# Kernel optimization log

Measured on AMD Instinct MI355X. Metric: run time of the kernel, lower is better.

## Reference

```python
import jax, jax.numpy as jnp
import numpy as np

DIM = 192
TDIM = 192
HEADS = 6
WS = (2, 7, 7)
SS = (1, 3, 3)
MLP_HID = 4 * DIM
RANK = DIM // 8
EPS = 1e-6


def _rel_pos_index(ws):
    wd, wh, ww = ws
    coords = np.stack(np.meshgrid(np.arange(wd), np.arange(wh), np.arange(ww), indexing='ij'))
    cf = coords.reshape(3, -1)
    rel = (cf[:, :, None] - cf[:, None, :]).transpose(1, 2, 0).astype(np.int64)
    rel[..., 0] += wd - 1
    rel[..., 1] += wh - 1
    rel[..., 2] += ww - 1
    rel[..., 0] *= (2 * wh - 1) * (2 * ww - 1)
    rel[..., 1] *= (2 * ww - 1)
    return rel.sum(-1)  # (N, N)


def _window_partition(x, ws):
    B, D, H, W, C = x.shape
    x = x.reshape(B, D // ws[0], ws[0], H // ws[1], ws[1], W // ws[2], ws[2], C)
    return x.transpose(0, 1, 3, 5, 2, 4, 6, 7).reshape(-1, ws[0] * ws[1] * ws[2], C)


def _window_reverse(w, ws, B, D, H, W):
    x = w.reshape(B, D // ws[0], H // ws[1], W // ws[2], ws[0], ws[1], ws[2], -1)
    return x.transpose(0, 1, 4, 2, 5, 3, 6, 7).reshape(B, D, H, W, -1)


def _ln(x):
    m = x.mean(-1, keepdims=True)
    v = ((x - m) ** 2).mean(-1, keepdims=True)
    return (x - m) * jax.lax.rsqrt(v + EPS)


def _compute_mask_np(Dp, Hp, Wp, ws, ss):
    img = np.zeros((1, Dp, Hp, Wp, 1), dtype=np.float32)
    cnt = 0
    for d in (slice(0, -ws[0]), slice(-ws[0], -ss[0]), slice(-ss[0], None)):
        for h in (slice(0, -ws[1]), slice(-ws[1], -ss[1]), slice(-ss[1], None)):
            for w in (slice(0, -ws[2]), slice(-ws[2], -ss[2]), slice(-ss[2], None)):
                img[:, d, h, w, :] = cnt
                cnt += 1
    x = img.reshape(1, Dp // ws[0], ws[0], Hp // ws[1], ws[1], Wp // ws[2], ws[2], 1)
    mw = x.transpose(0, 1, 3, 5, 2, 4, 6, 7).reshape(-1, ws[0] * ws[1] * ws[2])
    am = mw[:, None, :] - mw[:, :, None]
    return np.where(am != 0, np.float32(-100.0), np.float32(0.0))


def setup_inputs() -> dict:
    key = jax.random.key(0)
    ks = jax.random.split(key, 16)
    B, D, H, W, C = 1, 16, 64, 128, DIM
    Dp = D + (-D) % WS[0]
    Hp = H + (-H) % WS[1]
    Wp = W + (-W) % WS[2]
    s = 0.02
    bias_tab = (2 * WS[0] - 1) * (2 * WS[1] - 1) * (2 * WS[2] - 1)
    return {
        'x': jax.random.normal(ks[0], (B, D, H, W, C), jnp.float32),
        'mask_matrix': jnp.asarray(_compute_mask_np(Dp, Hp, Wp, WS, SS)),
        't': jax.random.normal(ks[1], (B, TDIM), jnp.float32),
        'w_qkv': jax.random.normal(ks[2], (C, 3 * C), jnp.float32) * s,
        'b_qkv': jnp.zeros((3 * C,), jnp.float32),
        'rel_bias': jax.random.normal(ks[3], (bias_tab, HEADS), jnp.float32) * s,
        'w_proj': jax.random.normal(ks[4], (C, C), jnp.float32) * s,
        'b_proj': jnp.zeros((C,), jnp.float32),
        'w1': jax.random.normal(ks[5], (C, MLP_HID), jnp.float32) * s,
        'b1': jnp.zeros((MLP_HID,), jnp.float32),
        'w2': jax.random.normal(ks[6], (MLP_HID, C), jnp.float32) * s,
        'b2': jnp.zeros((C,), jnp.float32),
        'wa1': jax.random.normal(ks[7], (TDIM, RANK), jnp.float32) * s,
        'wa2': jax.random.normal(ks[8], (RANK, 6 * C), jnp.float32) * s,
        'ba2': jax.random.normal(ks[9], (6 * C,), jnp.float32) * s,
    }


def reference(x, mask_matrix, t, w_qkv, b_qkv, rel_bias, w_proj, b_proj, w1, b1, w2, b2, wa1, wa2, ba2):
    B, D, H, W, C = x.shape
    hd = C // HEADS
    # AdaLN modulation params
    mod = (jax.nn.silu(t) @ wa1) @ wa2 + ba2  # (B, 6C)
    sh_msa, sc_msa, g_msa, sh_mlp, sc_mlp, g_mlp = jnp.split(mod, 6, axis=1)

    def modulate(y, sh, sc):
        return y * (1 + sc[:, None, None, None, :]) + sh[:, None, None, None, :]

    shortcut = x
    y = modulate(_ln(x), sh_msa, sc_msa)
    # pad to window multiples
    pad_d, pad_h, pad_w = (-D) % WS[0], (-H) % WS[1], (-W) % WS[2]
    y = jnp.pad(y, ((0, 0), (0, pad_d), (0, pad_h), (0, pad_w), (0, 0)))
    Dp, Hp, Wp = D + pad_d, H + pad_h, W + pad_w
    # cyclic shift
    y = jnp.roll(y, (-SS[0], -SS[1], -SS[2]), axis=(1, 2, 3))
    xw = _window_partition(y, WS)  # (B*nW, N, C)
    N = xw.shape[1]
    qkv = (xw @ w_qkv + b_qkv).reshape(-1, N, 3, HEADS, hd)
    q, k, v = qkv[:, :, 0], qkv[:, :, 1], qkv[:, :, 2]
    scale = hd ** -0.5
    attn = jnp.einsum('bnhd,bmhd->bhnm', q * scale, k)  # (B*nW, H, N, N)
    rpi = _rel_pos_index(WS)
    bias = rel_bias[rpi.reshape(-1)].reshape(N, N, HEADS).transpose(2, 0, 1)
    attn = attn + bias[None]
    nW = mask_matrix.shape[0]
    attn = attn.reshape(B, nW, HEADS, N, N) + mask_matrix[None, :, None]
    attn = jax.nn.softmax(attn, axis=-1).reshape(-1, HEADS, N, N)
    out = jnp.einsum('bhnm,bmhd->bnhd', attn, v).reshape(-1, N, C)
    out = out @ w_proj + b_proj
    y = _window_reverse(out, WS, B, Dp, Hp, Wp)
    y = jnp.roll(y, (SS[0], SS[1], SS[2]), axis=(1, 2, 3))
    y = y[:, :D, :H, :W, :]
    x1 = shortcut + g_msa[:, None, None, None, :] * y
    y2 = modulate(_ln(x1), sh_mlp, sc_mlp)
    h = jax.nn.gelu(y2 @ w1 + b1, approximate=False) @ w2 + b2
    return x1 + g_mlp[:, None, None, None, :] * h
```

## Files before the change

kernel.cpp:

```cpp
#include <hip/hip_runtime.h>
#include <hip/hip_bf16.h>

typedef __bf16 bf16x8 __attribute__((ext_vector_type(8)));
typedef float  f32x4  __attribute__((ext_vector_type(4)));
typedef unsigned int u32x4 __attribute__((ext_vector_type(4)));

__device__ inline unsigned short f2bf(float f) {
    union { __hip_bfloat16 h; unsigned short u; } cv;
    cv.h = __float2bfloat16(f);
    return cv.u;
}
__device__ inline float bf2f(unsigned short u) {
    union { unsigned int i; float f; } c; c.i = ((unsigned int)u) << 16; return c.f;
}

__device__ inline bf16x8 load8(const unsigned short* p) {
    uint2 lo = *(const uint2*)(p);
    uint2 hi = *(const uint2*)(p + 16);
    u32x4 v; v[0] = lo.x; v[1] = lo.y; v[2] = hi.x; v[3] = hi.y;
    return __builtin_bit_cast(bf16x8, v);
}

__device__ inline f32x4 mfma16(bf16x8 a, bf16x8 b, f32x4 c) {
    return __builtin_amdgcn_mfma_f32_16x16x32_bf16(a, b, c, 0, 0, 0);
}

__device__ inline bool winmapT(int gg, int& T) {
    int win = gg / 98, n = gg % 98;
    int wdi = win / 190, rem = win % 190, whi = rem / 19, wwi = rem % 19;
    int td = n / 49, th = (n / 7) % 7, tw = n % 7;
    int sd = (wdi * 2 + td + 1) & 15;
    int sh = whi * 7 + th + 3; if (sh >= 70) sh -= 70;
    int sw = wwi * 7 + tw + 3; if (sw >= 133) sw -= 133;
    if (sh < 64 && sw < 128) { T = (sd * 64 + sh) * 128 + sw; return true; }
    return false;
}

__global__ __launch_bounds__(256) void mod_k(const float* __restrict__ t,
    const float* __restrict__ wa1, const float* __restrict__ wa2,
    const float* __restrict__ ba2, float* __restrict__ mod)
{
    __shared__ float st[192];
    __shared__ float a[24];
    int tid = threadIdx.x;
    if (tid < 192) { float x = t[tid]; st[tid] = x / (1.f + __expf(-x)); }
    __syncthreads();
    if (tid < 24) {
        float s = 0.f;
        for (int c = 0; c < 192; ++c) s += st[c] * wa1[c * 24 + tid];
        a[tid] = s;
    }
    __syncthreads();
    for (int j = tid; j < 1152; j += 256) {
        float s = ba2[j];
        for (int r = 0; r < 24; ++r) s += a[r] * wa2[r * 1152 + j];
        mod[j] = s;
    }
}

__global__ __launch_bounds__(256) void prep_k(
    const float* __restrict__ wqkv, const float* __restrict__ wproj,
    const float* __restrict__ w1, const float* __restrict__ w2,
    const float* __restrict__ relb,
    unsigned short* __restrict__ wqkvT, unsigned short* __restrict__ wprojT,
    unsigned short* __restrict__ w1T, unsigned short* __restrict__ w2T,
    unsigned short* __restrict__ btabF)
{
    int i = blockIdx.x * 256 + threadIdx.x;
    if (i < 110592) { int n = i / 192, k = i % 192; wqkvT[i] = f2bf(wqkv[k * 576 + n]); return; }
    i -= 110592;
    if (i < 36864)  { int n = i / 192, k = i % 192; wprojT[i] = f2bf(wproj[k * 192 + n]); return; }
    i -= 36864;
    if (i < 147456) { int n = i / 192, k = i % 192; w1T[i] = f2bf(w1[k * 768 + n]); return; }
    i -= 147456;
    if (i < 147456) { int n = i / 768, k = i % 768; w2T[i] = f2bf(w2[k * 192 + n]); return; }
    i -= 147456;
    if (i < 688128) {
        int mt = i / 86016, r1 = i % 86016;
        int h  = r1 / 14336, r2 = r1 % 14336;
        int fm = r2 / 2048,  r3 = r2 % 2048;
        int le = r3 / 128,   r4 = r3 % 128;
        int l16 = r4 / 8,    fn = r4 % 8;
        int r = fm * 16 + le, c = fn * 16 + l16;
        float val;
        if (fn == 7 || r >= 98 || c >= 98) {
            val = -1e30f;
        } else {
            int tdn = r / 49, thn = (r / 7) % 7, twn = r % 7;
            int tdm = c / 49, thm = (c / 7) % 7, twm = c % 7;
            int idx = (tdn - tdm + 1) * 169 + (thn - thm + 6) * 13 + (twn - twm + 6);
            float b = relb[idx * 6 + h];
            int bd = mt & 1, bh = (mt >> 1) & 1, bw = (mt >> 2) & 1;
            int idn = (bd ? (tdn == 0 ? 1 : 2) : 0) * 9 + (bh ? (thn < 4 ? 1 : 2) : 0) * 3 + (bw ? (twn < 4 ? 1 : 2) : 0);
            int idm = (bd ? (tdm == 0 ? 1 : 2) : 0) * 9 + (bh ? (thm < 4 ? 1 : 2) : 0) * 3 + (bw ? (twm < 4 ? 1 : 2) : 0);
            val = b + ((idn != idm) ? -100.f : 0.f);
        }
        btabF[i] = f2bf(val);
    }
}

__global__ __launch_bounds__(256) void stats_f32_k(const float* __restrict__ x,
    float* __restrict__ st)
{
    int tok = blockIdx.x * 4 + (threadIdx.x >> 6);
    int lane = threadIdx.x & 63;
    const float* p = x + (size_t)tok * 192;
    float a = p[lane], b = p[64 + lane], c = p[128 + lane];
    float s = a + b + c, q = a * a + b * b + c * c;
    for (int m = 32; m; m >>= 1) { s += __shfl_xor(s, m); q += __shfl_xor(q, m); }
    if (lane == 0) {
        float mean = s * (1.f / 192.f);
        float var  = q * (1.f / 192.f) - mean * mean;
        st[2 * tok] = mean;
        st[2 * tok + 1] = rsqrtf(var + 1e-6f);
    }
}

template<int FN, int STAGE, int EPI>
__global__ __launch_bounds__(256) void gemm_k(
    const unsigned short* __restrict__ A, const float* __restrict__ Af,
    const unsigned short* __restrict__ BT, const float* __restrict__ bias,
    unsigned short* __restrict__ outB, float* outF,
    const float* __restrict__ auxF, const float* __restrict__ stats,
    const float* __restrict__ mod, int row0, int M, int N, int K)
{
    constexpr int BN = FN * 32;
    __shared__ unsigned short As[128][44];
    __shared__ unsigned short Bs[BN][44];
    const int t = threadIdx.x;
    const int n0 = blockIdx.x * BN, m0 = blockIdx.y * 128;
    const int lr = t >> 2, lk = (t & 3) * 8;
    const int wid = t >> 6, lane = t & 63;
    const int lg = lane >> 4, l16 = lane & 15;
    const int wm = (wid >> 1) * 64, wn = (wid & 1) * (FN * 16);
    f32x4 acc[4][FN] = {};

    float mn[2] = {0.f, 0.f}, rs[2] = {0.f, 0.f};
    size_t sbase[2] = {0, 0};
    bool va[2] = {false, false};
    #pragma unroll
    for (int rr = 0; rr < 2; ++rr) {
        int g = m0 + lr + rr * 64;
        if (STAGE == 1) {
            int T;
            if (g < M && winmapT(row0 + g, T)) {
                va[rr] = true; sbase[rr] = (size_t)T * 192;
                mn[rr] = stats[2 * T]; rs[rr] = stats[2 * T + 1];
            }
        } else if (STAGE == 2) {
            int tok = row0 + g;
            sbase[rr] = (size_t)tok * 192;
            mn[rr] = stats[2 * tok]; rs[rr] = stats[2 * tok + 1];
        }
    }

    for (int kk = 0; kk < K; kk += 32) {
        #pragma unroll
        for (int rr = 0; rr < 2; ++rr) {
            int r = lr + rr * 64;
            int g = m0 + r;
            uint4 w = make_uint4(0u, 0u, 0u, 0u);
            if (STAGE == 0) {
                if (g < M) w = *(const uint4*)(A + (size_t)g * K + kk + lk);
            } else if (STAGE == 1) {
                if (va[rr]) {
                    float4 xa = *(const float4*)(Af + sbase[rr] + kk + lk);
                    float4 xb = *(const float4*)(Af + sbase[rr] + kk + lk + 4);
                    float xs[8] = {xa.x, xa.y, xa.z, xa.w, xb.x, xb.y, xb.z, xb.w};
                    unsigned short o[8];
                    #pragma unroll
                    for (int j = 0; j < 8; ++j) {
                        int c = kk + lk + j;
                        o[j] = f2bf((xs[j] - mn[rr]) * rs[rr] * (1.f + mod[192 + c]) + mod[c]);
                    }
                    w = make_uint4((unsigned)o[0] | ((unsigned)o[1] << 16), (unsigned)o[2] | ((unsigned)o[3] << 16),
                                   (unsigned)o[4] | ((unsigned)o[5] << 16), (unsigned)o[6] | ((unsigned)o[7] << 16));
                }
            } else {
                float4 xa = *(const float4*)(Af + sbase[rr] + kk + lk);
                float4 xb = *(const float4*)(Af + sbase[rr] + kk + lk + 4);
                float xs[8] = {xa.x, xa.y, xa.z, xa.w, xb.x, xb.y, xb.z, xb.w};
                unsigned short o[8];
                #pragma unroll
                for (int j = 0; j < 8; ++j) {
                    int c = kk + lk + j;
                    o[j] = f2bf((xs[j] - mn[rr]) * rs[rr] * (1.f + mod[768 + c]) + mod[576 + c]);
                }
                w = make_uint4((unsigned)o[0] | ((unsigned)o[1] << 16), (unsigned)o[2] | ((unsigned)o[3] << 16),
                               (unsigned)o[4] | ((unsigned)o[5] << 16), (unsigned)o[6] | ((unsigned)o[7] << 16));
            }
            *(uint2*)(&As[r][lk])     = make_uint2(w.x, w.y);
            *(uint2*)(&As[r][lk + 4]) = make_uint2(w.z, w.w);
        }
        #pragma unroll
        for (int rr = 0; rr < BN / 64; ++rr) {
            int r = lr + rr * 64;
            int gn = n0 + r;
            uint4 w = make_uint4(0u, 0u, 0u, 0u);
            if (gn < N) w = *(const uint4*)(BT + (size_t)gn * K + kk + lk);
            *(uint2*)(&Bs[r][lk])     = make_uint2(w.x, w.y);
            *(uint2*)(&Bs[r][lk + 4]) = make_uint2(w.z, w.w);
        }
        __syncthreads();
        bf16x8 af[4], bv[FN];
        #pragma unroll
        for (int i = 0; i < 4; ++i) af[i] = load8(&As[wm + i * 16 + l16][4 * lg]);
        #pragma unroll
        for (int j = 0; j < FN; ++j) bv[j] = load8(&Bs[wn + j * 16 + l16][4 * lg]);
        #pragma unroll
        for (int i = 0; i < 4; ++i)
        #pragma unroll
        for (int j = 0; j < FN; ++j)
            acc[i][j] = mfma16(af[i], bv[j], acc[i][j]);
        __syncthreads();
    }

    #pragma unroll
    for (int i = 0; i < 4; ++i)
    #pragma unroll
    for (int j = 0; j < FN; ++j) {
        int gcol = n0 + wn + j * 16 + l16;
        if (gcol >= N) continue;
        float b = bias[gcol];
        #pragma unroll
        for (int e = 0; e < 4; ++e) {
            int grow = m0 + wm + i * 16 + lg * 4 + e;
            if (grow >= M) continue;
            float v = acc[i][j][e] + b;
            if (EPI == 0) {
                outB[(size_t)grow * N + gcol] = f2bf(v);
            } else if (EPI == 1) {
                float gl = 0.5f * v * (1.f + erff(v * 0.70710678118654752f));
                outB[(size_t)grow * N + gcol] = f2bf(gl);
            } else if (EPI == 2) {
                int T;
                if (winmapT(row0 + grow, T)) {
                    size_t idx = (size_t)T * 192 + gcol;
                    outF[idx] = auxF[idx] + mod[384 + gcol] * v;
                }
            } else {
                size_t idx = (size_t)(row0 + grow) * 192 + gcol;
                outF[idx] = outF[idx] + mod[960 + gcol] * v;
            }
        }
    }
}

__global__ __launch_bounds__(256) void attn_k(
    const unsigned short* __restrict__ qkv, const unsigned short* __restrict__ btabF,
    unsigned short* __restrict__ out)
{
    __shared__ __align__(16) char smem[40896];
    unsigned short* Qs  = (unsigned short*)smem;
    unsigned short* Ks  = (unsigned short*)(smem + 9856);
    unsigned short* Pbf = (unsigned short*)smem;
    unsigned short* VT  = (unsigned short*)(smem + 31808);

    const int blk = blockIdx.x;
    const int win = blk / 6, h = blk % 6;
    const int t = threadIdx.x;
    const int wid = t >> 6, lg = (t >> 4) & 3, l16 = t & 15;
    const size_t rb = (size_t)win * 98;

    const int wdi = win / 190, remw = win % 190, whi = remw / 19, wwi = remw % 19;
    const int mt = (wdi == 7 ? 1 : 0) | (whi == 9 ? 2 : 0) | (wwi == 18 ? 4 : 0);
    const unsigned short* btF = btabF + (size_t)(mt * 6 + h) * 14336;

    uint4 vreg[2];
    const int vi0 = t, vi1 = t + 256;
    if (vi0 < 392) vreg[0] = *(const uint4*)(qkv + (rb + (vi0 >> 2)) * 576 + 384 + h * 32 + (vi0 & 3) * 8);
    if (vi1 < 392) vreg[1] = *(const uint4*)(qkv + (rb + (vi1 >> 2)) * 576 + 384 + h * 32 + (vi1 & 3) * 8);

    for (int i = t; i < 98 * 4; i += 256) {
        int r = i >> 2, cg = (i & 3) * 8;
        uint4 q = *(const uint4*)(qkv + (rb + r) * 576 + h * 32 + cg);
        uint4 k = *(const uint4*)(qkv + (rb + r) * 576 + 192 + h * 32 + cg);
        *(uint2*)(Qs + r * 44 + cg)     = make_uint2(q.x, q.y);
        *(uint2*)(Qs + r * 44 + cg + 4) = make_uint2(q.z, q.w);
        *(uint2*)(Ks + r * 44 + cg)     = make_uint2(k.x, k.y);
        *(uint2*)(Ks + r * 44 + cg + 4) = make_uint2(k.z, k.w);
    }
    for (int i = t; i < 14 * 32; i += 256) {
        int r = 98 + (i >> 5), c = i & 31;
        Qs[r * 44 + c] = 0; Ks[r * 44 + c] = 0;
    }
    __syncthreads();

    f32x4 acc[2][7];
    {
        bf16x8 kb[7];
        #pragma unroll
        for (int fn = 0; fn < 7; ++fn) kb[fn] = load8(Ks + (fn * 16 + l16) * 44 + 4 * lg);
        #pragma unroll
        for (int fi = 0; fi < 2; ++fi) {
            int fm = wid + fi * 4;
            if (fm < 7) {
                bf16x8 qa = load8(Qs + (fm * 16 + l16) * 44 + 4 * lg);
                #pragma unroll
                for (int fn = 0; fn < 7; ++fn) {
                    f32x4 z = {};
                    acc[fi][fn] = mfma16(qa, kb[fn], z);
                }
            }
        }
    }
    __syncthreads();

    uint4 btreg[2][4];
    #pragma unroll
    for (int fi = 0; fi < 2; ++fi) {
        int fm = wid + fi * 4;
        int fmc = (fm < 7) ? fm : 0;
        #pragma unroll
        for (int e = 0; e < 4; ++e)
            btreg[fi][e] = *(const uint4*)(btF + fmc * 2048 + (lg * 4 + e) * 128 + l16 * 8);
    }
    {
        if (vi0 < 392) {
            int m = vi0 >> 2, c0 = (vi0 & 3) * 8;
            const unsigned short* vp = (const unsigned short*)&vreg[0];
            #pragma unroll
            for (int j = 0; j < 8; ++j) VT[(c0 + j) * 142 + m] = vp[j];
        }
        if (vi1 < 392) {
            int m = vi1 >> 2, c0 = (vi1 & 3) * 8;
            const unsigned short* vp = (const unsigned short*)&vreg[1];
            #pragma unroll
            for (int j = 0; j < 8; ++j) VT[(c0 + j) * 142 + m] = vp[j];
        }
    }
    for (int i = t; i < 32 * 30; i += 256) { int c = i / 30, m = 98 + i % 30; VT[c * 142 + m] = 0; }
    for (int i = t; i < 112 * 8; i += 256) {
        int r = i >> 3, cc = 112 + (i & 7) * 2;
        *(unsigned int*)(Pbf + r * 142 + cc) = 0u;
    }

    const float SCALE = 0.17677669529663687f;
    float rinv[2][4];
    #pragma unroll
    for (int fi = 0; fi < 2; ++fi) {
        int fm = wid + fi * 4;
        if (fm < 7) {
            #pragma unroll
            for (int e = 0; e < 4; ++e) {
                const unsigned int bw[4] = {btreg[fi][e].x, btreg[fi][e].y, btreg[fi][e].z, btreg[fi][e].w};
                float mx = -1e30f;
                #pragma unroll
                for (int fn = 0; fn < 7; ++fn) {
                    unsigned short bu = (unsigned short)(bw[fn >> 1] >> ((fn & 1) * 16));
                    float s = fmaf(acc[fi][fn][e], SCALE, bf2f(bu));
                    acc[fi][fn][e] = s;
                    mx = fmaxf(mx, s);
                }
                #pragma unroll
                for (int m = 1; m < 16; m <<= 1) mx = fmaxf(mx, __shfl_xor(mx, m));
                float sum = 0.f;
                #pragma unroll
                for (int fn = 0; fn < 7; ++fn) {
                    float p = __expf(acc[fi][fn][e] - mx);
                    acc[fi][fn][e] = p;
                    sum += p;
                }
                #pragma unroll
                for (int m = 1; m < 16; m <<= 1) sum += __shfl_xor(sum, m);
                rinv[fi][e] = 1.f / sum;
            }
            #pragma unroll
            for (int fn = 0; fn < 7; ++fn) {
                int c = fn * 16 + l16;
                #pragma unroll
                for (int e = 0; e < 4; ++e) {
                    int r = fm * 16 + lg * 4 + e;
                    Pbf[r * 142 + c] = f2bf(acc[fi][fn][e]);
                }
            }
        }
    }
    __syncthreads();

    #pragma unroll
    for (int fi = 0; fi < 2; ++fi) {
        int fm = wid + fi * 4;
        if (fm < 7) {
            bf16x8 sa[4];
            #pragma unroll
            for (int ks = 0; ks < 4; ++ks)
                sa[ks] = load8(Pbf + (fm * 16 + l16) * 142 + ks * 32 + 4 * lg);
            #pragma unroll
            for (int fn = 0; fn < 2; ++fn) {
                f32x4 o = {};
                #pragma unroll
                for (int ks = 0; ks < 4; ++ks) {
                    bf16x8 vb = load8(VT + (fn * 16 + l16) * 142 + ks * 32 + 4 * lg);
                    o = mfma16(sa[ks], vb, o);
                }
                #pragma unroll
                for (int e = 0; e < 4; ++e) {
                    int r = fm * 16 + lg * 4 + e;
                    if (r < 98) {
                        out[(rb + r) * 192 + h * 32 + fn * 16 + l16] = f2bf(o[e] * rinv[fi][e]);
                    }
                }
            }
        }
    }
}

extern "C" void kernel_launch(void* const* d_in, const int* in_sizes, int n_in,
                              void* d_out, int out_size, void* d_ws, size_t ws_size,
                              hipStream_t stream)
{
    const float* x      = (const float*)d_in[0];
    const float* tvec   = (const float*)d_in[2];
    const float* w_qkv  = (const float*)d_in[3];
    const float* b_qkv  = (const float*)d_in[4];
    const float* relb   = (const float*)d_in[5];
    const float* w_proj = (const float*)d_in[6];
    const float* b_proj = (const float*)d_in[7];
    const float* w1     = (const float*)d_in[8];
    const float* b1     = (const float*)d_in[9];
    const float* w2     = (const float*)d_in[10];
    const float* b2     = (const float*)d_in[11];
    const float* wa1    = (const float*)d_in[12];
    const float* wa2    = (const float*)d_in[13];
    const float* ba2    = (const float*)d_in[14];

    char* ws = (char*)d_ws;
    float*          mod    = (float*)ws;
    float*          stats1 = (float*)(ws + 4608);
    float*          stats2 = (float*)(ws + 1053184);
    unsigned short* wqkvT  = (unsigned short*)(ws + 2101760);
    unsigned short* wprojT = (unsigned short*)(ws + 2322944);
    unsigned short* w1T    = (unsigned short*)(ws + 2396672);
    unsigned short* w2T    = (unsigned short*)(ws + 2691584);
    unsigned short* btabF  = (unsigned short*)(ws + 2986496);
    unsigned short* qkvb   = (unsigned short*)(ws + 4834304);
    unsigned short* h      = (unsigned short*)(ws + 4834304);
    unsigned short* attn_c = (unsigned short*)(ws + 176436224);
    float*          dout   = (float*)d_out;

    mod_k<<<1, 256, 0, stream>>>(tvec, wa1, wa2, ba2, mod);
    prep_k<<<4416, 256, 0, stream>>>(w_qkv, w_proj, w1, w2, relb, wqkvT, wprojT, w1T, w2T, btabF);
    stats_f32_k<<<32768, 256, 0, stream>>>(x, stats1);

    gemm_k<4, 1, 0><<<dim3(5, 1164), 256, 0, stream>>>(
        nullptr, x, wqkvT, b_qkv, qkvb, nullptr, nullptr, stats1, mod, 0, 148960, 576, 192);
    attn_k<<<9120, 256, 0, stream>>>(qkvb, btabF, attn_c);
    gemm_k<2, 0, 2><<<dim3(3, 1164), 256, 0, stream>>>(
        attn_c, nullptr, wprojT, b_proj, nullptr, dout, x, nullptr, mod, 0, 148960, 192, 192);

    stats_f32_k<<<32768, 256, 0, stream>>>(dout, stats2);

    gemm_k<4, 2, 1><<<dim3(6, 1024), 256, 0, stream>>>(
        nullptr, dout, w1T, b1, h, nullptr, nullptr, stats2, mod, 0, 131072, 768, 192);
    gemm_k<2, 0, 3><<<dim3(3, 1024), 256, 0, stream>>>(
        h, nullptr, w2T, b2, nullptr, dout, nullptr, nullptr, mod, 0, 131072, 192, 768);
}
```

Before: 1.020 ms.

## Compute transposed QK^T so softmax probs feed PV MFMA directly from registers

The attention kernel now computes S^T = K·Q^T, so each lane holds scores for one query across keys. The accumulator layout then matches the A-operand layout of the PV MFMA, and P is packed straight into bf16 registers instead of going through a shared-memory round trip. This removes the P buffer, two __syncthreads and the row-wise shuffle reductions. The bias table is reordered to match the new layout, and the Q/K pitch changes to 46. The V transpose store is moved before the first barrier, which gives up the earlier overlap of the V load with QK compute.

```diff
diff --git a/kernel.cpp b/kernel.cpp
--- a/kernel.cpp
+++ b/kernel.cpp
@@ -78,16 +78,17 @@
     if (i < 688128) {
         int mt = i / 86016, r1 = i % 86016;
         int h  = r1 / 14336, r2 = r1 % 14336;
-        int fm = r2 / 2048,  r3 = r2 % 2048;
-        int le = r3 / 128,   r4 = r3 % 128;
-        int l16 = r4 / 8,    fn = r4 % 8;
-        int r = fm * 16 + le, c = fn * 16 + l16;
+        int fq = r2 / 2048,  r3 = r2 % 2048;
+        int l16 = r3 / 128,  r4 = r3 % 128;
+        int lg  = r4 / 32,   r5 = r4 % 32;
+        int fkey = r5 / 4,   e  = r5 % 4;
+        int q = fq * 16 + l16, key = fkey * 16 + lg * 4 + e;
         float val;
-        if (fn == 7 || r >= 98 || c >= 98) {
+        if (fkey == 7 || q >= 98 || key >= 98) {
             val = -1e30f;
         } else {
-            int tdn = r / 49, thn = (r / 7) % 7, twn = r % 7;
-            int tdm = c / 49, thm = (c / 7) % 7, twm = c % 7;
+            int tdn = q / 49, thn = (q / 7) % 7, twn = q % 7;
+            int tdm = key / 49, thm = (key / 7) % 7, twm = key % 7;
             int idx = (tdn - tdm + 1) * 169 + (thn - thm + 6) * 13 + (twn - twm + 6);
             float b = relb[idx * 6 + h];
             int bd = mt & 1, bh = (mt >> 1) & 1, bw = (mt >> 2) & 1;
@@ -250,11 +251,9 @@
     const unsigned short* __restrict__ qkv, const unsigned short* __restrict__ btabF,
     unsigned short* __restrict__ out)
 {
-    __shared__ __align__(16) char smem[40896];
-    unsigned short* Qs  = (unsigned short*)smem;
-    unsigned short* Ks  = (unsigned short*)(smem + 9856);
-    unsigned short* Pbf = (unsigned short*)smem;
-    unsigned short* VT  = (unsigned short*)(smem + 31808);
+    __shared__ __align__(16) unsigned short Qs[112 * 46];
+    __shared__ __align__(16) unsigned short Ks[112 * 46];
+    __shared__ __align__(16) unsigned short VT[32 * 142];
 
     const int blk = blockIdx.x;
     const int win = blk / 6, h = blk % 6;
@@ -266,140 +265,115 @@
     const int mt = (wdi == 7 ? 1 : 0) | (whi == 9 ? 2 : 0) | (wwi == 18 ? 4 : 0);
     const unsigned short* btF = btabF + (size_t)(mt * 6 + h) * 14336;
 
-    uint4 vreg[2];
-    const int vi0 = t, vi1 = t + 256;
-    if (vi0 < 392) vreg[0] = *(const uint4*)(qkv + (rb + (vi0 >> 2)) * 576 + 384 + h * 32 + (vi0 & 3) * 8);
-    if (vi1 < 392) vreg[1] = *(const uint4*)(qkv + (rb + (vi1 >> 2)) * 576 + 384 + h * 32 + (vi1 & 3) * 8);
-
     for (int i = t; i < 98 * 4; i += 256) {
         int r = i >> 2, cg = (i & 3) * 8;
         uint4 q = *(const uint4*)(qkv + (rb + r) * 576 + h * 32 + cg);
         uint4 k = *(const uint4*)(qkv + (rb + r) * 576 + 192 + h * 32 + cg);
-        *(uint2*)(Qs + r * 44 + cg)     = make_uint2(q.x, q.y);
-        *(uint2*)(Qs + r * 44 + cg + 4) = make_uint2(q.z, q.w);
-        *(uint2*)(Ks + r * 44 + cg)     = make_uint2(k.x, k.y);
-        *(uint2*)(Ks + r * 44 + cg + 4) = make_uint2(k.z, k.w);
+        *(uint2*)(Qs + r * 46 + cg)     = make_uint2(q.x, q.y);
+        *(uint2*)(Qs + r * 46 + cg + 4) = make_uint2(q.z, q.w);
+        *(uint2*)(Ks + r * 46 + cg)     = make_uint2(k.x, k.y);
+        *(uint2*)(Ks + r * 46 + cg + 4) = make_uint2(k.z, k.w);
     }
     for (int i = t; i < 14 * 32; i += 256) {
         int r = 98 + (i >> 5), c = i & 31;
-        Qs[r * 44 + c] = 0; Ks[r * 44 + c] = 0;
-    }
+        Qs[r * 46 + c] = 0; Ks[r * 46 + c] = 0;
+    }
+    if (t < 392) {
+        uint4 v = *(const uint4*)(qkv + (rb + (t >> 2)) * 576 + 384 + h * 32 + (t & 3) * 8);
+        const unsigned short* vp = (const unsigned short*)&v;
+        int m = t >> 2, c0 = (t & 3) * 8;
+        #pragma unroll
+        for (int j = 0; j < 8; ++j) VT[(c0 + j) * 142 + m] = vp[j];
+    }
+    {
+        int t2 = t + 256;
+        if (t2 < 392) {
+            uint4 v = *(const uint4*)(qkv + (rb + (t2 >> 2)) * 576 + 384 + h * 32 + (t2 & 3) * 8);
+            const unsigned short* vp = (const unsigned short*)&v;
+            int m = t2 >> 2, c0 = (t2 & 3) * 8;
+            #pragma unroll
+            for (int j = 0; j < 8; ++j) VT[(c0 + j) * 142 + m] = vp[j];
+        }
+    }
+    for (int i = t; i < 32 * 30; i += 256) { int c = i / 30, m = 98 + i % 30; VT[c * 142 + m] = 0; }
     __syncthreads();
 
-    f32x4 acc[2][7];
-    {
-        bf16x8 kb[7];
-        #pragma unroll
-        for (int fn = 0; fn < 7; ++fn) kb[fn] = load8(Ks + (fn * 16 + l16) * 44 + 4 * lg);
-        #pragma unroll
-        for (int fi = 0; fi < 2; ++fi) {
-            int fm = wid + fi * 4;
-            if (fm < 7) {
-                bf16x8 qa = load8(Qs + (fm * 16 + l16) * 44 + 4 * lg);
-                #pragma unroll
-                for (int fn = 0; fn < 7; ++fn) {
-                    f32x4 z = {};
-                    acc[fi][fn] = mfma16(qa, kb[fn], z);
-                }
-            }
-        }
-    }
-    __syncthreads();
-
-    uint4 btreg[2][4];
+    const float SCALE = 0.17677669529663687f;
     #pragma unroll
     for (int fi = 0; fi < 2; ++fi) {
-        int fm = wid + fi * 4;
-        int fmc = (fm < 7) ? fm : 0;
-        #pragma unroll
-        for (int e = 0; e < 4; ++e)
-            btreg[fi][e] = *(const uint4*)(btF + fmc * 2048 + (lg * 4 + e) * 128 + l16 * 8);
-    }
-    {
-        if (vi0 < 392) {
-            int m = vi0 >> 2, c0 = (vi0 & 3) * 8;
-            const unsigned short* vp = (const unsigned short*)&vreg[0];
+        const int fq = wid + fi * 4;
+        if (fq >= 7) break;
+
+        const uint4* bp = (const uint4*)(btF + fq * 2048 + l16 * 128 + lg * 32);
+        uint4 b0 = bp[0], b1 = bp[1], b2 = bp[2], b3 = bp[3];
+        const unsigned bt32[16] = {b0.x, b0.y, b0.z, b0.w, b1.x, b1.y, b1.z, b1.w,
+                                   b2.x, b2.y, b2.z, b2.w, b3.x, b3.y, b3.z, b3.w};
+
+        bf16x8 qa = load8(Qs + (fq * 16 + l16) * 46 + 4 * lg);
+        f32x4 acc[7];
+        #pragma unroll
+        for (int fk = 0; fk < 7; ++fk) {
+            bf16x8 kb = load8(Ks + (fk * 16 + l16) * 46 + 4 * lg);
+            f32x4 z = {};
+            acc[fk] = mfma16(kb, qa, z);
+        }
+
+        float mx = -1e30f;
+        #pragma unroll
+        for (int fk = 0; fk < 7; ++fk)
+        #pragma unroll
+        for (int e = 0; e < 4; ++e) {
+            unsigned short bu = (unsigned short)(bt32[fk * 2 + (e >> 1)] >> ((e & 1) * 16));
+            float s = fmaf(acc[fk][e], SCALE, bf2f(bu));
+            acc[fk][e] = s;
+            mx = fmaxf(mx, s);
+        }
+        mx = fmaxf(mx, __shfl_xor(mx, 16));
+        mx = fmaxf(mx, __shfl_xor(mx, 32));
+        float sum = 0.f;
+        #pragma unroll
+        for (int fk = 0; fk < 7; ++fk)
+        #pragma unroll
+        for (int e = 0; e < 4; ++e) {
+            float p = __expf(acc[fk][e] - mx);
+            acc[fk][e] = p;
+            sum += p;
+        }
+        sum += __shfl_xor(sum, 16);
+        sum += __shfl_xor(sum, 32);
+        float rinv = 1.f / sum;
+
+        bf16x8 sa[4];
+        #pragma unroll
+        for (int ks = 0; ks < 4; ++ks) {
+            u32x4 w;
+            w[0] = (unsigned)f2bf(acc[2 * ks][0]) | ((unsigned)f2bf(acc[2 * ks][1]) << 16);
+            w[1] = (unsigned)f2bf(acc[2 * ks][2]) | ((unsigned)f2bf(acc[2 * ks][3]) << 16);
+            if (ks < 3) {
+                w[2] = (unsigned)f2bf(acc[2 * ks + 1][0]) | ((unsigned)f2bf(acc[2 * ks + 1][1]) << 16);
+                w[3] = (unsigned)f2bf(acc[2 * ks + 1][2]) | ((unsigned)f2bf(acc[2 * ks + 1][3]) << 16);
+            } else {
+                w[2] = 0u; w[3] = 0u;
+            }
+            sa[ks] = __builtin_bit_cast(bf16x8, w);
+        }
+        float rv[4];
+        #pragma unroll
+        for (int e = 0; e < 4; ++e) rv[e] = __shfl(rinv, lg * 4 + e);
+
+        #pragma unroll
+        for (int fn = 0; fn < 2; ++fn) {
+            f32x4 o = {};
             #pragma unroll
-            for (int j = 0; j < 8; ++j) VT[(c0 + j) * 142 + m] = vp[j];
-        }
-        if (vi1 < 392) {
-            int m = vi1 >> 2, c0 = (vi1 & 3) * 8;
-            const unsigned short* vp = (const unsigned short*)&vreg[1];
-            #pragma unroll
-            for (int j = 0; j < 8; ++j) VT[(c0 + j) * 142 + m] = vp[j];
-        }
-    }
-    for (int i = t; i < 32 * 30; i += 256) { int c = i / 30, m = 98 + i % 30; VT[c * 142 + m] = 0; }
-    for (int i = t; i < 112 * 8; i += 256) {
-        int r = i >> 3, cc = 112 + (i & 7) * 2;
-        *(unsigned int*)(Pbf + r * 142 + cc) = 0u;
-    }
-
-    const float SCALE = 0.17677669529663687f;
-    float rinv[2][4];
-    #pragma unroll
-    for (int fi = 0; fi < 2; ++fi) {
-        int fm = wid + fi * 4;
-        if (fm < 7) {
+            for (int ks = 0; ks < 4; ++ks) {
+                bf16x8 vb = load8(VT + (fn * 16 + l16) * 142 + ks * 32 + 4 * lg);
+                o = mfma16(sa[ks], vb, o);
+            }
             #pragma unroll
             for (int e = 0; e < 4; ++e) {
-                const unsigned int bw[4] = {btreg[fi][e].x, btreg[fi][e].y, btreg[fi][e].z, btreg[fi][e].w};
-                float mx = -1e30f;
-                #pragma unroll
-                for (int fn = 0; fn < 7; ++fn) {
-                    unsigned short bu = (unsigned short)(bw[fn >> 1] >> ((fn & 1) * 16));
-                    float s = fmaf(acc[fi][fn][e], SCALE, bf2f(bu));
-                    acc[fi][fn][e] = s;
-                    mx = fmaxf(mx, s);
-                }
-                #pragma unroll
-                for (int m = 1; m < 16; m <<= 1) mx = fmaxf(mx, __shfl_xor(mx, m));
-                float sum = 0.f;
-                #pragma unroll
-                for (int fn = 0; fn < 7; ++fn) {
-                    float p = __expf(acc[fi][fn][e] - mx);
-                    acc[fi][fn][e] = p;
-                    sum += p;
-                }
-                #pragma unroll
-                for (int m = 1; m < 16; m <<= 1) sum += __shfl_xor(sum, m);
-                rinv[fi][e] = 1.f / sum;
-            }
-            #pragma unroll
-            for (int fn = 0; fn < 7; ++fn) {
-                int c = fn * 16 + l16;
-                #pragma unroll
-                for (int e = 0; e < 4; ++e) {
-                    int r = fm * 16 + lg * 4 + e;
-                    Pbf[r * 142 + c] = f2bf(acc[fi][fn][e]);
-                }
-            }
-        }
-    }
-    __syncthreads();
-
-    #pragma unroll
-    for (int fi = 0; fi < 2; ++fi) {
-        int fm = wid + fi * 4;
-        if (fm < 7) {
-            bf16x8 sa[4];
-            #pragma unroll
-            for (int ks = 0; ks < 4; ++ks)
-                sa[ks] = load8(Pbf + (fm * 16 + l16) * 142 + ks * 32 + 4 * lg);
-            #pragma unroll
-            for (int fn = 0; fn < 2; ++fn) {
-                f32x4 o = {};
-                #pragma unroll
-                for (int ks = 0; ks < 4; ++ks) {
-                    bf16x8 vb = load8(VT + (fn * 16 + l16) * 142 + ks * 32 + 4 * lg);
-                    o = mfma16(sa[ks], vb, o);
-                }
-                #pragma unroll
-                for (int e = 0; e < 4; ++e) {
-                    int r = fm * 16 + lg * 4 + e;
-                    if (r < 98) {
-                        out[(rb + r) * 192 + h * 32 + fn * 16 + l16] = f2bf(o[e] * rinv[fi][e]);
-                    }
+                int r = fq * 16 + lg * 4 + e;
+                if (r < 98) {
+                    out[(rb + r) * 192 + h * 32 + fn * 16 + l16] = f2bf(o[e] * rv[e]);
                 }
             }
         }
```

Result: no change. 1.016 ms (-0.4%).
